# Kernel optimization log

Measured on AMD Instinct MI355X. Metric: run time of the kernel, lower is better.

## Reference

```python
import jax, jax.numpy as jnp
import numpy as np

K = 1  # Op(k=1): num = num_op // k == num_op, so random.sample selects ALL ops (deterministic)


def setup_inputs() -> dict:
    key = jax.random.key(0)
    k1, k2, k3, k4, k5 = jax.random.split(key, 5)
    N, D = 50000, 128
    NUM_OP, E = 8, 400000
    return {
        "x": jax.random.normal(k1, (N, D), dtype=jnp.float32),
        "edge_vals": jax.random.uniform(k2, (NUM_OP, E), dtype=jnp.float32),
        "ws": jax.random.uniform(k3, (NUM_OP,), dtype=jnp.float32),
        "edge_rows": jax.random.randint(k4, (NUM_OP, E), 0, N, dtype=jnp.int32),
        "edge_cols": jax.random.randint(k5, (NUM_OP, E), 0, N, dtype=jnp.int32),
    }


def reference(x, edge_vals, ws, edge_rows, edge_cols):
    # out = (1/num) * sum_i ws[i] * spmm(A_i, x), with num = num_op (k=1 -> all ops sampled)
    N = x.shape[0]
    num_op = ws.shape[0]
    num = num_op // K
    out = jnp.zeros_like(x)
    for i in range(num_op):  # small fixed set of ops (NAS mixture), not a data dim
        msg = edge_vals[i][:, None] * x[edge_cols[i]]  # [E, D] gather + scale
        out = out + ws[i] * jax.ops.segment_sum(msg, edge_rows[i], num_segments=N)
    return out / num
```

## Files before the change

kernel.cpp:

```cpp
#include <hip/hip_runtime.h>


#define D_DIM 128
#define RPB_SHIFT 5
#define RPB 32
#define CSEG 8
#define CSEG_SHIFT 13
#define NB (RPB * CSEG)
#define MAXB 2048
#define CHUNK 8192
#define SCAN_BLOCK 1024
#define CVT_BLOCKS 1024
#define CNT_BLOCKS 256

typedef unsigned long long ull;

static __device__ __forceinline__ unsigned short f2bf(float f) {
    unsigned int u = __float_as_uint(f);
    u += 0x7FFFu + ((u >> 16) & 1u);
    return (unsigned short)(u >> 16);
}

static __device__ __forceinline__ ull pack2f(float a, float b) {
    return (ull)__float_as_uint(a) | ((ull)__float_as_uint(b) << 32);
}

__global__ __launch_bounds__(256) void spmm_scatter_kernel(
    const float* __restrict__ x, const float* __restrict__ edge_vals,
    const float* __restrict__ ws, const int* __restrict__ edge_rows,
    const int* __restrict__ edge_cols, float* __restrict__ out,
    int E, float inv_num)
{
    const int  op   = blockIdx.y;
    const long base = (long)op * (long)E;
    const float wscale = ws[op] * inv_num;
    const int lane = threadIdx.x & 63;
    const int wave = blockIdx.x * (blockDim.x >> 6) + (threadIdx.x >> 6);
    const int nwaves = gridDim.x * (blockDim.x >> 6);
    for (int e = wave; e < E; e += nwaves) {
        const int row = edge_rows[base + e];
        const int col = edge_cols[base + e];
        const float v = edge_vals[base + e] * wscale;
        const float2 xv = *reinterpret_cast<const float2*>(x + (long)col * D_DIM + lane * 2);
        float* o = out + (long)row * D_DIM + lane * 2;
        atomicAdd(o, xv.x * v);
        atomicAdd(o + 1, xv.y * v);
    }
}

__global__ __launch_bounds__(256) void convert_count_kernel(
    const float4* __restrict__ x4, ull* __restrict__ xh, int n4,
    const int* __restrict__ rows, int* __restrict__ gcount, long n, int B)
{
    __shared__ int h[MAXB];
    if (blockIdx.x < CVT_BLOCKS) {
        const int stride = CVT_BLOCKS * 256;
        for (int i = blockIdx.x * 256 + threadIdx.x; i < n4; i += stride) {
            const float4 v = x4[i];
            const ull p =
                (ull)f2bf(v.x)
                | ((ull)f2bf(v.y) << 16)
                | ((ull)f2bf(v.z) << 32)
                | ((ull)f2bf(v.w) << 48);
            xh[i] = p;
        }
    } else {
        const int cb = blockIdx.x - CVT_BLOCKS;
        for (int i = threadIdx.x; i < B; i += 256) h[i] = 0;
        __syncthreads();
        const long n4r = n >> 2;
        for (long q = (long)cb * 256 + threadIdx.x; q < n4r;
             q += (long)CNT_BLOCKS * 256) {
            const int4 r = reinterpret_cast<const int4*>(rows)[q];
            atomicAdd(&h[r.x >> RPB_SHIFT], 1);
            atomicAdd(&h[r.y >> RPB_SHIFT], 1);
            atomicAdd(&h[r.z >> RPB_SHIFT], 1);
            atomicAdd(&h[r.w >> RPB_SHIFT], 1);
        }
        if (cb == 0 && (long)threadIdx.x < (n & 3))
            atomicAdd(&h[rows[(n4r << 2) + threadIdx.x] >> RPB_SHIFT], 1);
        __syncthreads();
        for (int i = threadIdx.x; i < B; i += 256)
            if (h[i]) atomicAdd(&gcount[i], h[i]);
    }
}

__global__ __launch_bounds__(SCAN_BLOCK) void scan_kernel(
    int* __restrict__ cursors, int* __restrict__ offsets, int N)
{
    __shared__ int sdata[SCAN_BLOCK];
    __shared__ int carry_s;
    if (threadIdx.x == 0) carry_s = 0;
    __syncthreads();
    for (int base = 0; base < N; base += SCAN_BLOCK) {
        const int i = base + (int)threadIdx.x;
        const int v = (i < N) ? cursors[i] : 0;
        sdata[threadIdx.x] = v;
        __syncthreads();
        for (int ofs = 1; ofs < SCAN_BLOCK; ofs <<= 1) {
            int t = (threadIdx.x >= (unsigned)ofs) ? sdata[threadIdx.x - ofs] : 0;
            __syncthreads();
            sdata[threadIdx.x] += t;
            __syncthreads();
        }
        const int incl  = sdata[threadIdx.x];
        const int carry = carry_s;
        if (i < N) {
            const int excl = carry + incl - v;
            offsets[i] = excl;
            cursors[i] = excl;
        }
        __syncthreads();
        if (threadIdx.x == SCAN_BLOCK - 1) carry_s = carry + incl;
        __syncthreads();
    }
    if (threadIdx.x == 0) offsets[N] = carry_s;
}

__global__ __launch_bounds__(1024, 8) void scatter_bucket_kernel(
    const int* __restrict__ edge_rows, const int* __restrict__ edge_cols,
    const float* __restrict__ edge_vals, const float* __restrict__ ws,
    int* __restrict__ gcursor, ull* __restrict__ records,
    int E, float inv_num, int B)
{
    __shared__ int hist[MAXB];
    const int  op   = blockIdx.y;
    const long base = (long)op * (long)E;
    const int  e0   = blockIdx.x * CHUNK;
    const int  e1   = min(e0 + CHUNK, E);
    const float wscale = ws[op] * inv_num;
    const int  tid  = (int)threadIdx.x;
    const int*   erow = edge_rows + base;
    const int*   ecol = edge_cols + base;
    const float* eval = edge_vals + base;

    for (int i = tid; i < B; i += 1024) hist[i] = 0;
    __syncthreads();

    const int gA = e0 + tid * 4;
    const int gB = gA + 4096;
    int4 rA = make_int4(0, 0, 0, 0), rB = make_int4(0, 0, 0, 0);
    int  mA = 0, mB = 0;

    { const int rem = e1 - gA;
      if (rem >= 4) { rA = *reinterpret_cast<const int4*>(erow + gA); mA = 4; }
      else if (rem > 0) { mA = rem; rA.x = erow[gA];
          if (rem > 1) rA.y = erow[gA + 1];
          if (rem > 2) rA.z = erow[gA + 2]; } }
    { const int rem = e1 - gB;
      if (rem >= 4) { rB = *reinterpret_cast<const int4*>(erow + gB); mB = 4; }
      else if (rem > 0) { mB = rem; rB.x = erow[gB];
          if (rem > 1) rB.y = erow[gB + 1];
          if (rem > 2) rB.z = erow[gB + 2]; } }

    if (mA > 0) atomicAdd(&hist[rA.x >> RPB_SHIFT], 1);
    if (mA > 1) atomicAdd(&hist[rA.y >> RPB_SHIFT], 1);
    if (mA > 2) atomicAdd(&hist[rA.z >> RPB_SHIFT], 1);
    if (mA > 3) atomicAdd(&hist[rA.w >> RPB_SHIFT], 1);
    if (mB > 0) atomicAdd(&hist[rB.x >> RPB_SHIFT], 1);
    if (mB > 1) atomicAdd(&hist[rB.y >> RPB_SHIFT], 1);
    if (mB > 2) atomicAdd(&hist[rB.z >> RPB_SHIFT], 1);
    if (mB > 3) atomicAdd(&hist[rB.w >> RPB_SHIFT], 1);
    __syncthreads();

    for (int i = tid; i < B; i += 1024) {
        const int c = hist[i];
        hist[i] = c ? atomicAdd(&gcursor[i], c) : 0;
    }
    __syncthreads();

#define EMIT(RW, CW, VW)                                                       \
    { const int bin_ = (RW) >> RPB_SHIFT;                                      \
      const int pos_ = atomicAdd(&hist[bin_], 1);                              \
      const ull rec_ = ((ull)__float_as_uint((VW) * wscale) << 32)             \
          | ((unsigned int)((RW) & (RPB - 1)) << 16) | (unsigned int)(CW);     \
      records[pos_] = rec_; }

    if (mA > 0) {
        int4 c = make_int4(0, 0, 0, 0); float4 v = make_float4(0.f, 0.f, 0.f, 0.f);
        if (mA == 4) { c = *reinterpret_cast<const int4*>(ecol + gA);
                       v = *reinterpret_cast<const float4*>(eval + gA); }
        else { c.x = ecol[gA]; v.x = eval[gA];
               if (mA > 1) { c.y = ecol[gA + 1]; v.y = eval[gA + 1]; }
               if (mA > 2) { c.z = ecol[gA + 2]; v.z = eval[gA + 2]; } }
        EMIT(rA.x, c.x, v.x)
        if (mA > 1) EMIT(rA.y, c.y, v.y)
        if (mA > 2) EMIT(rA.z, c.z, v.z)
        if (mA > 3) EMIT(rA.w, c.w, v.w)
    }
    if (mB > 0) {
        int4 c = make_int4(0, 0, 0, 0); float4 v = make_float4(0.f, 0.f, 0.f, 0.f);
        if (mB == 4) { c = *reinterpret_cast<const int4*>(ecol + gB);
                       v = *reinterpret_cast<const float4*>(eval + gB); }
        else { c.x = ecol[gB]; v.x = eval[gB];
               if (mB > 1) { c.y = ecol[gB + 1]; v.y = eval[gB + 1]; }
               if (mB > 2) { c.z = ecol[gB + 2]; v.z = eval[gB + 2]; } }
        EMIT(rB.x, c.x, v.x)
        if (mB > 1) EMIT(rB.y, c.y, v.y)
        if (mB > 2) EMIT(rB.z, c.z, v.z)
        if (mB > 3) EMIT(rB.w, c.w, v.w)
    }
#undef EMIT
}

__global__ __launch_bounds__(512) void sort_bucket_kernel(
    const ull* __restrict__ records, unsigned int* __restrict__ sorted32,
    const int* __restrict__ boff, int* __restrict__ binoff, int N, int B)
{
    __shared__ int h[NB];
    __shared__ int cur[NB];
    __shared__ int wsum[4];
    __shared__ int woff[4];
    const int bkt   = blockIdx.x;
    const int start = boff[bkt], end = boff[bkt + 1];
    const int tid   = (int)threadIdx.x;
    const int lane  = tid & 63;
    const int w     = tid >> 6;

    if (tid < NB) h[tid] = 0;
    __syncthreads();
    for (int i = start + tid; i < end; i += 512) {
        const unsigned int lo = (unsigned int)records[i];
        const int bin = (int)((lo >> 16) << 3) | (int)((lo & 0xFFFFu) >> CSEG_SHIFT);
        atomicAdd(&h[bin], 1);
    }
    __syncthreads();
    if (tid < NB) {
        const int v = h[tid];
        int incl = v;
        #pragma unroll
        for (int o = 1; o < 64; o <<= 1) {
            const int t = __shfl_up(incl, o);
            if (lane >= o) incl += t;
        }
        if (lane == 63) wsum[w] = incl;
        __syncthreads();
        if (tid == 0) {
            int run = 0;
            #pragma unroll
            for (int k = 0; k < 4; ++k) { woff[k] = run; run += wsum[k]; }
        }
        __syncthreads();
        const int excl = start + woff[w] + incl - v;
        cur[tid] = excl;
        binoff[bkt * NB + tid] = excl;
    } else {
        __syncthreads();
        __syncthreads();
    }
    if (tid == 0 && bkt == B - 1) binoff[B * NB] = end;
    __syncthreads();
    for (int i = start + tid; i < end; i += 512) {
        const ull r = records[i];
        const unsigned int lo = (unsigned int)r;
        const int bin = (int)((lo >> 16) << 3) | (int)((lo & 0xFFFFu) >> CSEG_SHIFT);
        const int pos = atomicAdd(&cur[bin], 1);
        sorted32[pos] = (lo & 0xFFFFu)
            | ((unsigned int)f2bf(__uint_as_float((unsigned int)(r >> 32))) << 16);
    }
}

#define GREC(RK)                                                               \
    { const unsigned int p_ = *reinterpret_cast<const unsigned int*>(          \
          xh + (size_t)((RK)&0xFFFFu) * D_DIM + lane * 2);                     \
      const float v_ = __uint_as_float((RK)&0xFFFF0000u);                      \
      ax += v_ * __uint_as_float(p_ << 16);                                    \
      ay += v_ * __uint_as_float(p_ & 0xFFFF0000u); }

__global__ __launch_bounds__(512) void gather_seg_kernel(
    const unsigned short* __restrict__ xh, const int* __restrict__ binoff,
    const unsigned int* __restrict__ sorted32, float* __restrict__ out,
    int N, int B)
{
    const int tid  = (int)threadIdx.x;
    const int lane = tid & 63;
    const int w    = tid >> 6;
    const int bkt  = blockIdx.x * 2 + (w >> 2);
    if (bkt >= B) return;
    const int rl0  = (w & 3) * 8;
    const int bb   = bkt * NB + rl0 * CSEG;

    float accx[8], accy[8];
    int jcur[8];
    #pragma unroll
    for (int rr = 0; rr < 8; ++rr) {
        accx[rr] = 0.f; accy[rr] = 0.f;
        jcur[rr] = __builtin_amdgcn_readfirstlane(binoff[bb + rr * CSEG]);
    }

    for (int seg = 0; seg < CSEG; ++seg) {
        int jend[8];
        #pragma unroll
        for (int rr = 0; rr < 8; ++rr)
            jend[rr] = __builtin_amdgcn_readfirstlane(
                binoff[bb + rr * CSEG + seg + 1]);
        #pragma unroll
        for (int rr = 0; rr < 8; ++rr) {
            int j = jcur[rr];
            const int je = jend[rr];
            float ax = accx[rr], ay = accy[rr];
            for (; j + 7 < je; j += 8) {
                const unsigned int r0 = sorted32[j];
                const unsigned int r1 = sorted32[j + 1];
                const unsigned int r2 = sorted32[j + 2];
                const unsigned int r3 = sorted32[j + 3];
                const unsigned int r4 = sorted32[j + 4];
                const unsigned int r5 = sorted32[j + 5];
                const unsigned int r6 = sorted32[j + 6];
                const unsigned int r7 = sorted32[j + 7];
                GREC(r0) GREC(r1) GREC(r2) GREC(r3)
                GREC(r4) GREC(r5) GREC(r6) GREC(r7)
            }
            if (j + 3 < je) {
                const unsigned int r0 = sorted32[j];
                const unsigned int r1 = sorted32[j + 1];
                const unsigned int r2 = sorted32[j + 2];
                const unsigned int r3 = sorted32[j + 3];
                GREC(r0) GREC(r1) GREC(r2) GREC(r3)
                j += 4;
            }
            if (j + 1 < je) {
                const unsigned int r0 = sorted32[j];
                const unsigned int r1 = sorted32[j + 1];
                GREC(r0) GREC(r1)
                j += 2;
            }
            if (j < je) {
                const unsigned int r0 = sorted32[j];
                GREC(r0)
            }
            accx[rr] = ax; accy[rr] = ay;
            jcur[rr] = je;
        }
    }

    const int row0 = (bkt << RPB_SHIFT) + rl0;
    #pragma unroll
    for (int rr = 0; rr < 8; ++rr) {
        const int row = row0 + rr;
        if (row < N)
            __builtin_nontemporal_store(pack2f(accx[rr], accy[rr]),
                reinterpret_cast<ull*>(out + (size_t)row * D_DIM + lane * 2));
    }
}

__global__ __launch_bounds__(1024) void gather_filter2_kernel(
    const unsigned short* __restrict__ xh, const int* __restrict__ boff,
    const ull* __restrict__ records, float* __restrict__ out, int N)
{
    const int lane = threadIdx.x & 63;
    const int wv   = threadIdx.x >> 6;
    const int bkt  = blockIdx.x;
    const int row0 = (bkt << RPB_SHIFT) + wv * 2;
    const int row1 = row0 + 1;
    const int start = boff[bkt], end = boff[bkt + 1];

    float a0x = 0.f, a0y = 0.f, a1x = 0.f, a1y = 0.f;
    for (int c = start; c < end; c += 64) {
        const int idx = c + lane;
        unsigned int lo = 0xFFFF0000u, hi = 0;
        if (idx < end) {
            const ull r = __builtin_nontemporal_load(&records[idx]);
            lo = (unsigned int)r;
            hi = (unsigned int)(r >> 32);
        }
        ull mask = __ballot((lo >> 17) == (unsigned int)wv);
        while (mask) {
            const int j = __ffsll(mask) - 1;
            mask &= mask - 1;
            const unsigned int lj = __shfl(lo, j);
            const float v = __uint_as_float(__shfl(hi, j));
            const unsigned int col = lj & 0xFFFFu;
            const unsigned int p = *reinterpret_cast<const unsigned int*>(
                xh + (size_t)col * D_DIM + lane * 2);
            const float px = __uint_as_float(p << 16);
            const float py = __uint_as_float(p & 0xFFFF0000u);
            if (lj & 0x10000u) { a1x += v * px; a1y += v * py; }
            else               { a0x += v * px; a0y += v * py; }
        }
    }
    if (row0 < N)
        __builtin_nontemporal_store(pack2f(a0x, a0y),
            reinterpret_cast<ull*>(out + (size_t)row0 * D_DIM + lane * 2));
    if (row1 < N)
        __builtin_nontemporal_store(pack2f(a1x, a1y),
            reinterpret_cast<ull*>(out + (size_t)row1 * D_DIM + lane * 2));
}

extern "C" void kernel_launch(void* const* d_in, const int* in_sizes, int n_in,
                              void* d_out, int out_size, void* d_ws, size_t ws_size,
                              hipStream_t stream)
{
    const float* x         = (const float*)d_in[0];
    const float* edge_vals = (const float*)d_in[1];
    const float* ws        = (const float*)d_in[2];
    const int*   edge_rows = (const int*)d_in[3];
    const int*   edge_cols = (const int*)d_in[4];
    float*       out       = (float*)d_out;

    const int num_op = in_sizes[2];
    const int E      = in_sizes[1] / num_op;
    const int N      = in_sizes[0] / D_DIM;
    const long Etot  = (long)num_op * (long)E;
    const int  B     = (N + RPB - 1) / RPB;
    const float inv_num = 1.0f / (float)num_op;

    const size_t off_boff    = 0;
    const size_t off_gcur    = ((size_t)(B + 1) * 4 + 255) & ~(size_t)255;
    const size_t off_binoff  = (off_gcur + (size_t)B * 4 + 255) & ~(size_t)255;
    const size_t off_xh      = (off_binoff + ((size_t)B * NB + 1) * 4 + 255) & ~(size_t)255;
    const size_t off_records = (off_xh + (size_t)N * D_DIM * 2 + 255) & ~(size_t)255;
    const size_t off_sorted  = off_records + (size_t)Etot * 8;
    const size_t need_sort   = off_sorted + (size_t)Etot * 4;
    const size_t need_filter = off_sorted;

    if (ws_size < need_filter || B > MAXB || N > 65535) {
        (void)hipMemsetAsync(d_out, 0, (size_t)out_size * sizeof(float), stream);
        dim3 grid(256, num_op, 1);
        spmm_scatter_kernel<<<grid, 256, 0, stream>>>(
            x, edge_vals, ws, edge_rows, edge_cols, out, E, inv_num);
        return;
    }

    int* boff    = (int*)((char*)d_ws + off_boff);
    int* gcursor = (int*)((char*)d_ws + off_gcur);
    int* binoff  = (int*)((char*)d_ws + off_binoff);
    unsigned short* xh = (unsigned short*)((char*)d_ws + off_xh);
    ull* records = (ull*)((char*)d_ws + off_records);
    unsigned int* sorted32 = (unsigned int*)((char*)d_ws + off_sorted);

    (void)hipMemsetAsync(gcursor, 0, (size_t)B * 4, stream);

    convert_count_kernel<<<CVT_BLOCKS + CNT_BLOCKS, 256, 0, stream>>>(
        (const float4*)x, (ull*)xh, N * D_DIM / 4, edge_rows, gcursor, Etot, B);
    scan_kernel<<<1, SCAN_BLOCK, 0, stream>>>(gcursor, boff, B);

    dim3 sgrid((E + CHUNK - 1) / CHUNK, num_op, 1);
    scatter_bucket_kernel<<<sgrid, 1024, 0, stream>>>(
        edge_rows, edge_cols, edge_vals, ws, gcursor, records, E, inv_num, B);

    if (ws_size >= need_sort) {
        sort_bucket_kernel<<<B, 512, 0, stream>>>(
            records, sorted32, boff, binoff, N, B);
        gather_seg_kernel<<<(B + 1) / 2, 512, 0, stream>>>(
            xh, binoff, sorted32, out, N, B);
    } else {
        gather_filter2_kernel<<<B, 1024, 0, stream>>>(xh, boff, records, out, N);
    }
}
```

Baseline: 176.1 us.

## Stage sorted edge records in LDS per column segment in gather kernel

The bin order inside each bucket changes from row-major to segment-major, so every column segment of a bucket occupies one contiguous range. The gather kernel then cooperatively copies each segment's records for two buckets into shared memory, and wavefronts read their rows' records from LDS instead of issuing scalar-broadcast global loads. Records beyond a capacity cap fall back to global reads. This adds two block-wide barriers per segment and removes the early exit for out-of-range buckets.

```diff
diff --git a/kernel.cpp b/kernel.cpp
--- a/kernel.cpp
+++ b/kernel.cpp
@@ -12,6 +12,7 @@
 #define SCAN_BLOCK 1024
 #define CVT_BLOCKS 1024
 #define CNT_BLOCKS 256
+#define SEGCAP 1024
 
 typedef unsigned long long ull;
 
@@ -221,7 +222,8 @@
     __syncthreads();
     for (int i = start + tid; i < end; i += 512) {
         const unsigned int lo = (unsigned int)records[i];
-        const int bin = (int)((lo >> 16) << 3) | (int)((lo & 0xFFFFu) >> CSEG_SHIFT);
+        const int bin = (int)(((lo & 0xFFFFu) >> CSEG_SHIFT) << RPB_SHIFT)
+                      | (int)(lo >> 16);
         atomicAdd(&h[bin], 1);
     }
     __syncthreads();
@@ -253,7 +255,8 @@
     for (int i = start + tid; i < end; i += 512) {
         const ull r = records[i];
         const unsigned int lo = (unsigned int)r;
-        const int bin = (int)((lo >> 16) << 3) | (int)((lo & 0xFFFFu) >> CSEG_SHIFT);
+        const int bin = (int)(((lo & 0xFFFFu) >> CSEG_SHIFT) << RPB_SHIFT)
+                      | (int)(lo >> 16);
         const int pos = atomicAdd(&cur[bin], 1);
         sorted32[pos] = (lo & 0xFFFFu)
             | ((unsigned int)f2bf(__uint_as_float((unsigned int)(r >> 32))) << 16);
@@ -272,65 +275,85 @@
     const unsigned int* __restrict__ sorted32, float* __restrict__ out,
     int N, int B)
 {
+    __shared__ unsigned int rbuf[2][SEGCAP];
     const int tid  = (int)threadIdx.x;
     const int lane = tid & 63;
     const int w    = tid >> 6;
-    const int bkt  = blockIdx.x * 2 + (w >> 2);
-    if (bkt >= B) return;
+    const int bkt0 = blockIdx.x * 2;
+    const int h    = w >> 2;
+    const int bkt  = bkt0 + h;
     const int rl0  = (w & 3) * 8;
-    const int bb   = bkt * NB + rl0 * CSEG;
+    const int nb1  = (bkt0 + 1 < B);
 
     float accx[8], accy[8];
-    int jcur[8];
     #pragma unroll
-    for (int rr = 0; rr < 8; ++rr) {
-        accx[rr] = 0.f; accy[rr] = 0.f;
-        jcur[rr] = __builtin_amdgcn_readfirstlane(binoff[bb + rr * CSEG]);
-    }
+    for (int rr = 0; rr < 8; ++rr) { accx[rr] = 0.f; accy[rr] = 0.f; }
 
     for (int seg = 0; seg < CSEG; ++seg) {
-        int jend[8];
-        #pragma unroll
-        for (int rr = 0; rr < 8; ++rr)
-            jend[rr] = __builtin_amdgcn_readfirstlane(
-                binoff[bb + rr * CSEG + seg + 1]);
-        #pragma unroll
-        for (int rr = 0; rr < 8; ++rr) {
-            int j = jcur[rr];
-            const int je = jend[rr];
-            float ax = accx[rr], ay = accy[rr];
-            for (; j + 7 < je; j += 8) {
-                const unsigned int r0 = sorted32[j];
-                const unsigned int r1 = sorted32[j + 1];
-                const unsigned int r2 = sorted32[j + 2];
-                const unsigned int r3 = sorted32[j + 3];
-                const unsigned int r4 = sorted32[j + 4];
-                const unsigned int r5 = sorted32[j + 5];
-                const unsigned int r6 = sorted32[j + 6];
-                const unsigned int r7 = sorted32[j + 7];
-                GREC(r0) GREC(r1) GREC(r2) GREC(r3)
-                GREC(r4) GREC(r5) GREC(r6) GREC(r7)
+        const int base0 = binoff[(size_t)bkt0 * NB + seg * RPB];
+        const int end0  = binoff[(size_t)bkt0 * NB + (seg + 1) * RPB];
+        const int len0  = min(end0 - base0, SEGCAP);
+        int base1 = 0, len1 = 0;
+        if (nb1) {
+            base1 = binoff[(size_t)(bkt0 + 1) * NB + seg * RPB];
+            const int end1 = binoff[(size_t)(bkt0 + 1) * NB + (seg + 1) * RPB];
+            len1 = min(end1 - base1, SEGCAP);
+        }
+        __syncthreads();
+        for (int i = tid; i < len0; i += 512) rbuf[0][i] = sorted32[base0 + i];
+        for (int i = tid; i < len1; i += 512) rbuf[1][i] = sorted32[base1 + i];
+        __syncthreads();
+
+        if (bkt < B) {
+            const int segbase = h ? base1 : base0;
+            const int seglen  = h ? len1 : len0;
+            const unsigned int* rb = rbuf[h];
+            const size_t bb = (size_t)bkt * NB + seg * RPB + rl0;
+            int ofs[9];
+            #pragma unroll
+            for (int rr = 0; rr < 9; ++rr)
+                ofs[rr] = __builtin_amdgcn_readfirstlane(binoff[bb + rr]) - segbase;
+            #pragma unroll
+            for (int rr = 0; rr < 8; ++rr) {
+                int j        = min(ofs[rr], seglen);
+                const int je = min(ofs[rr + 1], seglen);
+                float ax = accx[rr], ay = accy[rr];
+                for (; j + 7 < je; j += 8) {
+                    const unsigned int r0 = rb[j];
+                    const unsigned int r1 = rb[j + 1];
+                    const unsigned int r2 = rb[j + 2];
+                    const unsigned int r3 = rb[j + 3];
+                    const unsigned int r4 = rb[j + 4];
+                    const unsigned int r5 = rb[j + 5];
+                    const unsigned int r6 = rb[j + 6];
+                    const unsigned int r7 = rb[j + 7];
+                    GREC(r0) GREC(r1) GREC(r2) GREC(r3)
+                    GREC(r4) GREC(r5) GREC(r6) GREC(r7)
+                }
+                if (j + 3 < je) {
+                    const unsigned int r0 = rb[j];
+                    const unsigned int r1 = rb[j + 1];
+                    const unsigned int r2 = rb[j + 2];
+                    const unsigned int r3 = rb[j + 3];
+                    GREC(r0) GREC(r1) GREC(r2) GREC(r3)
+                    j += 4;
+                }
+                if (j + 1 < je) {
+                    const unsigned int r0 = rb[j];
+                    const unsigned int r1 = rb[j + 1];
+                    GREC(r0) GREC(r1)
+                    j += 2;
+                }
+                if (j < je) {
+                    const unsigned int r0 = rb[j];
+                    GREC(r0)
+                }
+                for (int g = max(ofs[rr], seglen); g < ofs[rr + 1]; ++g) {
+                    const unsigned int r0 = sorted32[segbase + g];
+                    GREC(r0)
+                }
+                accx[rr] = ax; accy[rr] = ay;
             }
-            if (j + 3 < je) {
-                const unsigned int r0 = sorted32[j];
-                const unsigned int r1 = sorted32[j + 1];
-                const unsigned int r2 = sorted32[j + 2];
-                const unsigned int r3 = sorted32[j + 3];
-                GREC(r0) GREC(r1) GREC(r2) GREC(r3)
-                j += 4;
-            }
-            if (j + 1 < je) {
-                const unsigned int r0 = sorted32[j];
-                const unsigned int r1 = sorted32[j + 1];
-                GREC(r0) GREC(r1)
-                j += 2;
-            }
-            if (j < je) {
-                const unsigned int r0 = sorted32[j];
-                GREC(r0)
-            }
-            accx[rr] = ax; accy[rr] = ay;
-            jcur[rr] = je;
         }
     }
 
@@ -338,7 +361,7 @@
     #pragma unroll
     for (int rr = 0; rr < 8; ++rr) {
         const int row = row0 + rr;
-        if (row < N)
+        if (bkt < B && row < N)
             __builtin_nontemporal_store(pack2f(accx[rr], accy[rr]),
                 reinterpret_cast<ull*>(out + (size_t)row * D_DIM + lane * 2));
     }
```

Result: slower. 195.8 us (+11.2%).
